# Kernel tuning notes

Measured on AMD Instinct MI355X. Metric: run time of the kernel, lower is better.

The kernel has to match this reference:

```python
import jax, jax.numpy as jnp
import numpy as np

HIDDEN = 1024
NUM_HEADS = 16
HEAD_DIM = HIDDEN // NUM_HEADS


def setup_inputs() -> dict:
    key = jax.random.key(0)
    ks = jax.random.split(key, 5)
    scale = 1.0 / np.sqrt(HIDDEN)
    x = jax.random.normal(ks[0], (2, 2048, HIDDEN), dtype=jnp.float32)
    qkv_w = jax.random.uniform(ks[1], (3 * HIDDEN, HIDDEN), jnp.float32, -scale, scale)
    qkv_b = jax.random.uniform(ks[2], (3 * HIDDEN,), jnp.float32, -scale, scale)
    out_w = jax.random.uniform(ks[3], (HIDDEN, HIDDEN), jnp.float32, -scale, scale)
    out_b = jax.random.uniform(ks[4], (HIDDEN,), jnp.float32, -scale, scale)
    return {"x": x, "qkv_w": qkv_w, "qkv_b": qkv_b, "out_w": out_w, "out_b": out_b}


def reference(x, qkv_w, qkv_b, out_w, out_b):
    B, S, _ = x.shape
    qkv = jnp.einsum('bsd,ed->bse', x, qkv_w) + qkv_b  # [B,S,3H]
    q, k, v = jnp.split(qkv, 3, axis=-1)
    # [B,S,H] -> [B,nh,S,hd]
    def to_heads(t):
        return t.reshape(B, S, NUM_HEADS, HEAD_DIM).transpose(0, 2, 1, 3)
    q, k, v = to_heads(q), to_heads(k), to_heads(v)
    scores = jnp.einsum('bhqd,bhkd->bhqk', q, k) / np.sqrt(HEAD_DIM).astype(np.float32)
    attn = jax.nn.softmax(scores, axis=-1)
    o = jnp.einsum('bhqk,bhkd->bhqd', attn, v)
    o = o.transpose(0, 2, 1, 3).reshape(B, S, HIDDEN)
    return jnp.einsum('bsd,ed->bse', o, out_w) + out_b
```

## Files before the change

kernel.cpp:

```cpp
#include <hip/hip_runtime.h>
#include <stdint.h>

typedef __bf16 bf16x8 __attribute__((ext_vector_type(8)));
typedef float  f32x4  __attribute__((ext_vector_type(4)));
typedef float  f32x16 __attribute__((ext_vector_type(16)));
typedef unsigned short u16;
typedef unsigned int   u32;

#define B_  2
#define S_  2048
#define H_  1024
#define NH_ 16
#define HD_ 64
#define QSCL 0.18033688011112042f

__device__ __forceinline__ u16 f2bf(float f) {
  u32 u = __builtin_bit_cast(u32, f);
  return (u16)((u + 0x7FFFu + ((u >> 16) & 1u)) >> 16);
}
__device__ __forceinline__ float ex2(float x) { return __builtin_amdgcn_exp2f(x); }
__device__ __forceinline__ u32 cvtpk(float lo, float hi) {
  u32 r; asm("v_cvt_pk_bf16_f32 %0, %1, %2" : "=v"(r) : "v"(lo), "v"(hi)); return r;
}
__device__ __forceinline__ void gload_lds16(const u16* g, u16* lds) {
  __builtin_amdgcn_global_load_lds(
      (__attribute__((address_space(1))) void*)(void*)g,
      (__attribute__((address_space(3))) void*)lds, 16, 0, 0);
}

__global__ void cvt_all(const float* __restrict__ a, const float* __restrict__ b,
                        const float* __restrict__ c, u16* __restrict__ oa,
                        u16* __restrict__ ob, u16* __restrict__ oc) {
  int i = blockIdx.x * 256 + threadIdx.x;
  const float4* src; ushort4* dst; int j;
  if (i < 1048576)      { src = (const float4*)a; dst = (ushort4*)oa; j = i; }
  else if (i < 1835008) { src = (const float4*)b; dst = (ushort4*)ob; j = i - 1048576; }
  else                  { src = (const float4*)c; dst = (ushort4*)oc; j = i - 1835008; }
  const float4 v = src[j];
  ushort4 o;
  o.x = f2bf(v.x); o.y = f2bf(v.y); o.z = f2bf(v.z); o.w = f2bf(v.w);
  dst[j] = o;
}

__global__ __launch_bounds__(256, 2)
void gemm_qkv(const u16* __restrict__ A, const u16* __restrict__ W,
              const float* __restrict__ bias,
              u16* __restrict__ qb, u16* __restrict__ kb, u16* __restrict__ vb,
              int M, int N, int K)
{
  __shared__ __align__(16) u16 As[2][128 * 32];
  __shared__ __align__(16) u16 Bs[2][128 * 32];
  const int tid = threadIdx.x;
  const int w = tid >> 6, l = tid & 63;
  const int lg = l >> 4, lr = l & 15;
  const int wr = w >> 1, wc = w & 1;
  const int tM = blockIdx.y * 128, tN = blockIdx.x * 128;

  f32x4 acc[4][4];
  const f32x4 z4 = {0.f, 0.f, 0.f, 0.f};
#pragma unroll
  for (int m = 0; m < 4; ++m)
#pragma unroll
    for (int n = 0; n < 4; ++n) acc[m][n] = z4;

  auto STG = [&](int buf, int k0) {
#pragma unroll
    for (int i = 0; i < 2; ++i) {
      const int ch = i * 256 + tid;
      const int row = ch >> 2, cc = (ch & 3) * 8;
      gload_lds16(A + (size_t)(tM + row) * K + k0 + cc, As[buf] + (size_t)(i * 256 + w * 64) * 8);
      gload_lds16(W + (size_t)(tN + row) * K + k0 + cc, Bs[buf] + (size_t)(i * 256 + w * 64) * 8);
    }
  };

  STG(0, 0);
  __syncthreads();

  for (int it = 0; it < K / 32; ++it) {
    const int cur = it & 1;
    if (it + 1 < K / 32) STG(cur ^ 1, (it + 1) * 32);
    bf16x8 af[4], bw[4];
#pragma unroll
    for (int m = 0; m < 4; ++m)
      af[m] = *(const bf16x8*)&As[cur][(wr * 64 + m * 16 + lr) * 32 + lg * 8];
#pragma unroll
    for (int n = 0; n < 4; ++n)
      bw[n] = *(const bf16x8*)&Bs[cur][(wc * 64 + n * 16 + lr) * 32 + lg * 8];
#pragma unroll
    for (int m = 0; m < 4; ++m)
#pragma unroll
      for (int n = 0; n < 4; ++n)
        acc[m][n] = __builtin_amdgcn_mfma_f32_16x16x32_bf16(af[m], bw[n], acc[m][n], 0, 0, 0);
    __syncthreads();
  }

#pragma unroll
  for (int n = 0; n < 4; ++n) {
    const int col = tN + wc * 64 + n * 16 + lr;
    const float bv = bias[col];
    const int t3 = col >> 10, rem = col & 1023;
    const int hh = rem >> 6, dd = rem & 63;
    const float sc = (t3 == 0) ? QSCL : 1.f;
    u16* dst = (t3 == 0) ? qb : (t3 == 1) ? kb : vb;
#pragma unroll
    for (int m = 0; m < 4; ++m)
#pragma unroll
      for (int r = 0; r < 4; ++r) {
        const int row = tM + wr * 64 + m * 16 + lg * 4 + r;
        const int bb = row >> 11, ss = row & 2047;
        dst[((size_t)(bb * NH_ + hh) * S_ + ss) * HD_ + dd] = f2bf((acc[m][n][r] + bv) * sc);
      }
  }
}

__global__ __launch_bounds__(256, 4)
void vtrans(const u16* __restrict__ vb, u16* __restrict__ vtb)
{
  __shared__ u16 Ls[64 * 65];
  const int t = threadIdx.x;
  const int bh = blockIdx.y;
  const int s0 = blockIdx.x * 64;
  const u16* src = vb + ((size_t)bh * S_ + s0) * HD_;
  const int d = t & 63, sy = t >> 6;
#pragma unroll
  for (int p = 0; p < 16; ++p) {
    const int s = p * 4 + sy;
    Ls[s * 65 + d] = src[(size_t)s * HD_ + d];
  }
  __syncthreads();
  const int s = t & 63, dy = t >> 6;
  u16* dst = vtb + (size_t)bh * HD_ * S_ + s0;
#pragma unroll
  for (int p = 0; p < 16; ++p) {
    const int dd = p * 4 + dy;
    dst[(size_t)dd * S_ + s] = Ls[s * 65 + dd];
  }
}

__global__ __launch_bounds__(256, 2)
void gemm_out(const u16* __restrict__ A, const u16* __restrict__ W,
              const float* __restrict__ bias, float* __restrict__ outf,
              int M, int N, int K)
{
  __shared__ __align__(16) u16 As[2][128 * 32];
  __shared__ __align__(16) u16 Bs[2][64 * 32];
  const int tid = threadIdx.x;
  const int w = tid >> 6, l = tid & 63;
  const int lg = l >> 4, lr = l & 15;
  const int tM = blockIdx.y * 128, tN = blockIdx.x * 64;

  f32x4 acc[2][4];
  const f32x4 z4 = {0.f, 0.f, 0.f, 0.f};
#pragma unroll
  for (int m = 0; m < 2; ++m)
#pragma unroll
    for (int n = 0; n < 4; ++n) acc[m][n] = z4;

  auto STG = [&](int buf, int k0) {
#pragma unroll
    for (int i = 0; i < 2; ++i) {
      const int ch = i * 256 + tid;
      const int row = ch >> 2, cc = (ch & 3) * 8;
      gload_lds16(A + (size_t)(tM + row) * K + k0 + cc, As[buf] + (size_t)(i * 256 + w * 64) * 8);
    }
    gload_lds16(W + (size_t)(tN + (tid >> 2)) * K + k0 + (tid & 3) * 8, Bs[buf] + (size_t)(w * 64) * 8);
  };

  STG(0, 0);
  __syncthreads();

  for (int it = 0; it < K / 32; ++it) {
    const int cur = it & 1;
    if (it + 1 < K / 32) STG(cur ^ 1, (it + 1) * 32);
    bf16x8 af[2], bw[4];
#pragma unroll
    for (int m = 0; m < 2; ++m)
      af[m] = *(const bf16x8*)&As[cur][(w * 32 + m * 16 + lr) * 32 + lg * 8];
#pragma unroll
    for (int n = 0; n < 4; ++n)
      bw[n] = *(const bf16x8*)&Bs[cur][(n * 16 + lr) * 32 + lg * 8];
#pragma unroll
    for (int m = 0; m < 2; ++m)
#pragma unroll
      for (int n = 0; n < 4; ++n)
        acc[m][n] = __builtin_amdgcn_mfma_f32_16x16x32_bf16(af[m], bw[n], acc[m][n], 0, 0, 0);
    __syncthreads();
  }

#pragma unroll
  for (int n = 0; n < 4; ++n) {
    const int col = tN + n * 16 + lr;
    const float bv = bias[col];
#pragma unroll
    for (int m = 0; m < 2; ++m)
#pragma unroll
      for (int r = 0; r < 4; ++r) {
        const int row = tM + w * 32 + m * 16 + lg * 4 + r;
        outf[(size_t)row * N + col] = acc[m][n][r] + bv;
      }
  }
}

__global__ __launch_bounds__(256, 2)
void attn_fwd(const u16* __restrict__ qb, const u16* __restrict__ kb,
              const u16* __restrict__ vtb, u16* __restrict__ ob)
{
  __shared__ __align__(16) u16 Kl[2][2][64 * 64];
  __shared__ __align__(16) u16 Vl[2][2][64 * 64];

  const int tid = threadIdx.x;
  const int w = tid >> 6, l = tid & 63;
  const int q32 = l & 31, hi = l >> 5;
  const int idx = blockIdx.x;
  const int bh = idx & 31, qt = idx >> 5;
  const int bb = bh >> 4, hh = bh & 15;
  const int q0 = qt * 128 + w * 32;

  bf16x8 qf[4];
#pragma unroll
  for (int ks = 0; ks < 4; ++ks)
    qf[ks] = *(const bf16x8*)&qb[((size_t)bh * S_ + q0 + q32) * HD_ + ks * 16 + hi * 8];

  const f32x16 z16 = {};
  f32x16 acc[2] = {z16, z16};
  float lrun = 0.f;

  const int srow = l >> 3;
  const int scol = ((l & 7) ^ srow) << 3;
  const u16* kbase = kb  + ((size_t)bh * S_  + w * 16 + srow) * HD_ + scol;
  const u16* vbase = vtb + ((size_t)bh * HD_ + w * 16 + srow) * S_  + scol;

  auto STAGE = [&](int buf, int t) {
#pragma unroll
    for (int s = 0; s < 2; ++s)
#pragma unroll
      for (int j = 0; j < 2; ++j) {
        gload_lds16(kbase + ((size_t)t * 128 + s * 64) * HD_ + j * 8 * HD_,
                    &Kl[buf][s][(w * 16 + j * 8) * 64]);
        gload_lds16(vbase + (size_t)t * 128 + s * 64 + j * 8 * S_,
                    &Vl[buf][s][(w * 16 + j * 8) * 64]);
      }
  };

  STAGE(0, 0);
  __syncthreads();

  const int sw = q32 & 7;

  auto SOFTMAX = [&](f32x16& st0, f32x16& st1, bf16x8* pa) {
#pragma unroll
    for (int kt = 0; kt < 2; ++kt) {
      const f32x16& stt = kt ? st1 : st0;
      float p[16];
#pragma unroll
      for (int r = 0; r < 16; ++r) p[r] = ex2(stt[r]);
#pragma unroll
      for (int g = 0; g < 4; ++g)
        lrun += (p[4 * g] + p[4 * g + 1]) + (p[4 * g + 2] + p[4 * g + 3]);
      u32 wk0[4], wk1[4];
#pragma unroll
      for (int g = 0; g < 4; ++g) {
        wk0[g] = cvtpk(p[4 * g], p[4 * g + 1]);
        wk1[g] = cvtpk(p[4 * g + 2], p[4 * g + 3]);
      }
#pragma unroll
      for (int k2 = 0; k2 < 2; ++k2) {
        u32 a0 = wk0[2 * k2], b0 = wk0[2 * k2 + 1];
        u32 a1 = wk1[2 * k2], b1 = wk1[2 * k2 + 1];
        asm volatile("v_permlane32_swap_b32 %0, %1" : "+v"(a0), "+v"(b0));
        asm volatile("v_permlane32_swap_b32 %0, %1" : "+v"(a1), "+v"(b1));
        uint4 wv = {a0, a1, b0, b1};
        pa[kt * 2 + k2] = __builtin_bit_cast(bf16x8, wv);
      }
    }
  };

  for (int t = 0; t < 16; ++t) {
    const int cur = t & 1;
    if (t + 1 < 16) STAGE(cur ^ 1, t + 1);

    f32x16 stA0 = z16, stA1 = z16, stB0 = z16, stB1 = z16;
    __builtin_amdgcn_s_setprio(1);
#pragma unroll
    for (int ks = 0; ks < 4; ++ks) {
      const int so = ((((ks << 1) | hi) ^ sw) << 3);
      const bf16x8 kfA0 = *(const bf16x8*)&Kl[cur][0][(q32) * 64 + so];
      const bf16x8 kfA1 = *(const bf16x8*)&Kl[cur][0][(32 + q32) * 64 + so];
      const bf16x8 kfB0 = *(const bf16x8*)&Kl[cur][1][(q32) * 64 + so];
      const bf16x8 kfB1 = *(const bf16x8*)&Kl[cur][1][(32 + q32) * 64 + so];
      stA0 = __builtin_amdgcn_mfma_f32_32x32x16_bf16(kfA0, qf[ks], stA0, 0, 0, 0);
      stA1 = __builtin_amdgcn_mfma_f32_32x32x16_bf16(kfA1, qf[ks], stA1, 0, 0, 0);
      stB0 = __builtin_amdgcn_mfma_f32_32x32x16_bf16(kfB0, qf[ks], stB0, 0, 0, 0);
      stB1 = __builtin_amdgcn_mfma_f32_32x32x16_bf16(kfB1, qf[ks], stB1, 0, 0, 0);
    }
    __builtin_amdgcn_s_setprio(0);

    bf16x8 pa[4];
    SOFTMAX(stA0, stA1, pa);
    __builtin_amdgcn_s_setprio(1);
#pragma unroll
    for (int dt = 0; dt < 2; ++dt)
#pragma unroll
      for (int ks = 0; ks < 4; ++ks) {
        const bf16x8 vf = *(const bf16x8*)&Vl[cur][0][(dt * 32 + q32) * 64 + ((((ks << 1) | hi) ^ sw) << 3)];
        acc[dt] = __builtin_amdgcn_mfma_f32_32x32x16_bf16(vf, pa[ks], acc[dt], 0, 0, 0);
      }
    __builtin_amdgcn_s_setprio(0);

    SOFTMAX(stB0, stB1, pa);
    __builtin_amdgcn_s_setprio(1);
#pragma unroll
    for (int dt = 0; dt < 2; ++dt)
#pragma unroll
      for (int ks = 0; ks < 4; ++ks) {
        const bf16x8 vf = *(const bf16x8*)&Vl[cur][1][(dt * 32 + q32) * 64 + ((((ks << 1) | hi) ^ sw) << 3)];
        acc[dt] = __builtin_amdgcn_mfma_f32_32x32x16_bf16(vf, pa[ks], acc[dt], 0, 0, 0);
      }
    __builtin_amdgcn_s_setprio(0);

    __syncthreads();
  }

  lrun += __shfl_xor(lrun, 32);
  const float linv = 1.f / lrun;
  const size_t orow = ((size_t)(bb * S_ + q0 + q32)) * H_ + hh * HD_;
#pragma unroll
  for (int dt = 0; dt < 2; ++dt)
#pragma unroll
    for (int g = 0; g < 4; ++g) {
      const u32 o0 = cvtpk(acc[dt][4 * g] * linv, acc[dt][4 * g + 1] * linv);
      const u32 o1 = cvtpk(acc[dt][4 * g + 2] * linv, acc[dt][4 * g + 3] * linv);
      uint2 ov; ov.x = o0; ov.y = o1;
      *(uint2*)&ob[orow + dt * 32 + g * 8 + hi * 4] = ov;
    }
}

extern "C" void kernel_launch(void* const* d_in, const int* in_sizes, int n_in,
                              void* d_out, int out_size, void* d_ws, size_t ws_size,
                              hipStream_t stream) {
  const float* x     = (const float*)d_in[0];
  const float* qkv_w = (const float*)d_in[1];
  const float* qkv_b = (const float*)d_in[2];
  const float* out_w = (const float*)d_in[3];
  const float* out_b = (const float*)d_in[4];

  char* ws = (char*)d_ws;
  u16* xb    = (u16*)(ws);
  u16* wqkvb = (u16*)(ws + 8388608);
  u16* wob   = (u16*)(ws + 14680064);
  u16* qb    = (u16*)(ws + 16777216);
  u16* kb    = (u16*)(ws + 25165824);
  u16* vb    = (u16*)(ws + 33554432);
  u16* ob    = (u16*)(ws + 41943040);
  u16* vtb   = xb;

  cvt_all<<<8192, 256, 0, stream>>>(x, qkv_w, out_w, xb, wqkvb, wob);

  gemm_qkv<<<dim3(24, 32), 256, 0, stream>>>(xb, wqkvb, qkv_b,
                                             qb, kb, vb, 4096, 3072, 1024);
  vtrans<<<dim3(32, 32), 256, 0, stream>>>(vb, vtb);
  attn_fwd<<<512, 256, 0, stream>>>(qb, kb, vtb, ob);
  gemm_out<<<dim3(16, 32), 256, 0, stream>>>(ob, wob, out_b, (float*)d_out,
                                             4096, 1024, 1024);
}
```

Before: 114.9 us.

## Restructure QKV GEMM with 256x192 tiles, XOR-swizzled LDS and interleaved prefetch

Rewrites the QKV projection GEMM to use 512-thread blocks computing 256x192 output tiles with a K-step of 64. The LDS layout is XOR-swizzled to avoid bank conflicts, and next-stage global->LDS loads are interleaved with the MFMA phases using raw s_barrier and s_setprio. The aim is more data reuse per tile, fewer LDS conflicts and better overlap of loads with math. The cost is more registers and LDS per block and a grid of 256 blocks, which may under-fill the CUs.

```diff
diff --git a/kernel.cpp b/kernel.cpp
--- a/kernel.cpp
+++ b/kernel.cpp
@@ -27,6 +27,7 @@
       (__attribute__((address_space(1))) void*)(void*)g,
       (__attribute__((address_space(3))) void*)lds, 16, 0, 0);
 }
+#define SBAR() asm volatile("s_barrier" ::: "memory")
 
 __global__ void cvt_all(const float* __restrict__ a, const float* __restrict__ b,
                         const float* __restrict__ c, u16* __restrict__ oa,
@@ -42,71 +43,100 @@
   dst[j] = o;
 }
 
-__global__ __launch_bounds__(256, 2)
+__global__ __launch_bounds__(512, 2)
 void gemm_qkv(const u16* __restrict__ A, const u16* __restrict__ W,
               const float* __restrict__ bias,
-              u16* __restrict__ qb, u16* __restrict__ kb, u16* __restrict__ vb,
-              int M, int N, int K)
+              u16* __restrict__ qb, u16* __restrict__ kb, u16* __restrict__ vb)
 {
-  __shared__ __align__(16) u16 As[2][128 * 32];
-  __shared__ __align__(16) u16 Bs[2][128 * 32];
+  __shared__ __align__(16) u16 Al[2][256 * 64];
+  __shared__ __align__(16) u16 Bl[2][192 * 64];
+  const int K = 1024;
   const int tid = threadIdx.x;
   const int w = tid >> 6, l = tid & 63;
   const int lg = l >> 4, lr = l & 15;
-  const int wr = w >> 1, wc = w & 1;
-  const int tM = blockIdx.y * 128, tN = blockIdx.x * 128;
-
-  f32x4 acc[4][4];
-  const f32x4 z4 = {0.f, 0.f, 0.f, 0.f};
-#pragma unroll
-  for (int m = 0; m < 4; ++m)
-#pragma unroll
-    for (int n = 0; n < 4; ++n) acc[m][n] = z4;
-
-  auto STG = [&](int buf, int k0) {
-#pragma unroll
-    for (int i = 0; i < 2; ++i) {
-      const int ch = i * 256 + tid;
-      const int row = ch >> 2, cc = (ch & 3) * 8;
-      gload_lds16(A + (size_t)(tM + row) * K + k0 + cc, As[buf] + (size_t)(i * 256 + w * 64) * 8);
-      gload_lds16(W + (size_t)(tN + row) * K + k0 + cc, Bs[buf] + (size_t)(i * 256 + w * 64) * 8);
-    }
-  };
-
-  STG(0, 0);
-  __syncthreads();
-
-  for (int it = 0; it < K / 32; ++it) {
-    const int cur = it & 1;
-    if (it + 1 < K / 32) STG(cur ^ 1, (it + 1) * 32);
-    bf16x8 af[4], bw[4];
-#pragma unroll
-    for (int m = 0; m < 4; ++m)
-      af[m] = *(const bf16x8*)&As[cur][(wr * 64 + m * 16 + lr) * 32 + lg * 8];
-#pragma unroll
-    for (int n = 0; n < 4; ++n)
-      bw[n] = *(const bf16x8*)&Bs[cur][(wc * 64 + n * 16 + lr) * 32 + lg * 8];
-#pragma unroll
-    for (int m = 0; m < 4; ++m)
-#pragma unroll
-      for (int n = 0; n < 4; ++n)
-        acc[m][n] = __builtin_amdgcn_mfma_f32_16x16x32_bf16(af[m], bw[n], acc[m][n], 0, 0, 0);
-    __syncthreads();
-  }
-
-#pragma unroll
-  for (int n = 0; n < 4; ++n) {
-    const int col = tN + wc * 64 + n * 16 + lr;
+  const int wm = w >> 2, wn = w & 3;
+  const int tM = blockIdx.y * 256, tN = blockIdx.x * 192;
+
+  f32x4 acc[8][3] = {};
+
+  const int srow = l >> 3;
+  const int scol = ((l & 7) ^ srow) << 3;
+  const u16* asrc = A + (size_t)(tM + w * 8 + srow) * K + scol;
+  const u16* bsrc = W + (size_t)(tN + w * 8 + srow) * K + scol;
+
+  auto STGA = [&](int buf, int k0, int j) {
+    gload_lds16(asrc + (size_t)j * 64 * K + k0, &Al[buf][(j * 64 + w * 8) * 64]);
+  };
+  auto STGB = [&](int buf, int k0, int j) {
+    gload_lds16(bsrc + (size_t)j * 64 * K + k0, &Bl[buf][(j * 64 + w * 8) * 64]);
+  };
+
+#pragma unroll
+  for (int j = 0; j < 4; ++j) STGA(0, 0, j);
+#pragma unroll
+  for (int j = 0; j < 3; ++j) STGB(0, 0, j);
+  asm volatile("s_waitcnt vmcnt(0)" ::: "memory");
+  SBAR();
+
+  const int sw = lr & 7;
+
+  for (int t = 0; t < 16; ++t) {
+    const int cur = t & 1, nb = cur ^ 1;
+    const int k1 = (t + 1) * 64;
+    const bool pre = (t + 1 < 16);
+
+    bf16x8 bw[3][2];
+
+#pragma unroll
+    for (int p = 0; p < 4; ++p) {
+      bf16x8 af[2][2];
+#pragma unroll
+      for (int m2 = 0; m2 < 2; ++m2)
+#pragma unroll
+        for (int kk = 0; kk < 2; ++kk)
+          af[m2][kk] = *(const bf16x8*)&Al[cur][(wm * 128 + (p * 2 + m2) * 16 + lr) * 64 +
+                                               (((kk * 4 + lg) ^ sw) << 3)];
+      if (p == 0) {
+#pragma unroll
+        for (int n = 0; n < 3; ++n)
+#pragma unroll
+          for (int kk = 0; kk < 2; ++kk)
+            bw[n][kk] = *(const bf16x8*)&Bl[cur][(wn * 48 + n * 16 + lr) * 64 +
+                                                (((kk * 4 + lg) ^ sw) << 3)];
+      }
+      if (pre) {
+        STGA(nb, k1, p);
+        if (p < 3) STGB(nb, k1, p);
+      }
+      SBAR();
+      __builtin_amdgcn_s_setprio(1);
+#pragma unroll
+      for (int m2 = 0; m2 < 2; ++m2)
+#pragma unroll
+        for (int n = 0; n < 3; ++n)
+#pragma unroll
+          for (int kk = 0; kk < 2; ++kk)
+            acc[p * 2 + m2][n] = __builtin_amdgcn_mfma_f32_16x16x32_bf16(
+                af[m2][kk], bw[n][kk], acc[p * 2 + m2][n], 0, 0, 0);
+      __builtin_amdgcn_s_setprio(0);
+      if (p == 3) asm volatile("s_waitcnt vmcnt(0)" ::: "memory");
+      SBAR();
+    }
+  }
+
+#pragma unroll
+  for (int n = 0; n < 3; ++n) {
+    const int col = tN + wn * 48 + n * 16 + lr;
     const float bv = bias[col];
     const int t3 = col >> 10, rem = col & 1023;
     const int hh = rem >> 6, dd = rem & 63;
     const float sc = (t3 == 0) ? QSCL : 1.f;
     u16* dst = (t3 == 0) ? qb : (t3 == 1) ? kb : vb;
 #pragma unroll
-    for (int m = 0; m < 4; ++m)
+    for (int m = 0; m < 8; ++m)
 #pragma unroll
       for (int r = 0; r < 4; ++r) {
-        const int row = tM + wr * 64 + m * 16 + lg * 4 + r;
+        const int row = tM + wm * 128 + m * 16 + lg * 4 + r;
         const int bb = row >> 11, ss = row & 2047;
         dst[((size_t)(bb * NH_ + hh) * S_ + ss) * HD_ + dd] = f2bf((acc[m][n][r] + bv) * sc);
       }
@@ -356,8 +386,7 @@
 
   cvt_all<<<8192, 256, 0, stream>>>(x, qkv_w, out_w, xb, wqkvb, wob);
 
-  gemm_qkv<<<dim3(24, 32), 256, 0, stream>>>(xb, wqkvb, qkv_b,
-                                             qb, kb, vb, 4096, 3072, 1024);
+  gemm_qkv<<<dim3(16, 16), 512, 0, stream>>>(xb, wqkvb, qkv_b, qb, kb, vb);
   vtrans<<<dim3(32, 32), 256, 0, stream>>>(vb, vtb);
   attn_fwd<<<512, 256, 0, stream>>>(qb, kb, vtb, ob);
   gemm_out<<<dim3(16, 32), 256, 0, stream>>>(ob, wob, out_b, (float*)d_out,
```

Result: no change. 114.9 us (+0.0%).

## Restructure QKV GEMM with 128x192x64 tiles, XOR-swizzled LDS and priority hints

Applied to the files above, without the earlier changes.

Reworks the QKV projection GEMM to use larger 128x192 output tiles with a 64-wide K step, halving the number of K iterations and barriers. LDS stores use an XOR swizzle on 16-byte chunks to avoid bank conflicts on fragment reads. Explicit vmcnt waits plus raw s_barrier replace __syncthreads, and s_setprio is raised around the MFMA block. The grid shrinks from 768 to 512 blocks, and each block uses more LDS and accumulator registers, which may lower occupancy.

```diff
diff --git a/kernel.cpp b/kernel.cpp
--- a/kernel.cpp
+++ b/kernel.cpp
@@ -27,6 +27,7 @@
       (__attribute__((address_space(1))) void*)(void*)g,
       (__attribute__((address_space(3))) void*)lds, 16, 0, 0);
 }
+#define SBAR() asm volatile("s_barrier" ::: "memory")
 
 __global__ void cvt_all(const float* __restrict__ a, const float* __restrict__ b,
                         const float* __restrict__ c, u16* __restrict__ oa,
@@ -45,58 +46,70 @@
 __global__ __launch_bounds__(256, 2)
 void gemm_qkv(const u16* __restrict__ A, const u16* __restrict__ W,
               const float* __restrict__ bias,
-              u16* __restrict__ qb, u16* __restrict__ kb, u16* __restrict__ vb,
-              int M, int N, int K)
+              u16* __restrict__ qb, u16* __restrict__ kb, u16* __restrict__ vb)
 {
-  __shared__ __align__(16) u16 As[2][128 * 32];
-  __shared__ __align__(16) u16 Bs[2][128 * 32];
+  __shared__ __align__(16) u16 Al[2][128 * 64];
+  __shared__ __align__(16) u16 Bl[2][192 * 64];
+  const int K = 1024;
   const int tid = threadIdx.x;
   const int w = tid >> 6, l = tid & 63;
   const int lg = l >> 4, lr = l & 15;
-  const int wr = w >> 1, wc = w & 1;
-  const int tM = blockIdx.y * 128, tN = blockIdx.x * 128;
-
-  f32x4 acc[4][4];
-  const f32x4 z4 = {0.f, 0.f, 0.f, 0.f};
-#pragma unroll
-  for (int m = 0; m < 4; ++m)
-#pragma unroll
-    for (int n = 0; n < 4; ++n) acc[m][n] = z4;
+  const int wm = w >> 1, wn = w & 1;
+  const int tM = blockIdx.y * 128, tN = blockIdx.x * 192;
+
+  f32x4 acc[4][6] = {};
+
+  const int srow = l >> 3;
+  const int scol = ((l & 7) ^ srow) << 3;
+  const u16* asrc = A + (size_t)(tM + w * 32 + srow) * K + scol;
+  const u16* bsrc = W + (size_t)(tN + w * 48 + srow) * K + scol;
 
   auto STG = [&](int buf, int k0) {
 #pragma unroll
-    for (int i = 0; i < 2; ++i) {
-      const int ch = i * 256 + tid;
-      const int row = ch >> 2, cc = (ch & 3) * 8;
-      gload_lds16(A + (size_t)(tM + row) * K + k0 + cc, As[buf] + (size_t)(i * 256 + w * 64) * 8);
-      gload_lds16(W + (size_t)(tN + row) * K + k0 + cc, Bs[buf] + (size_t)(i * 256 + w * 64) * 8);
-    }
+    for (int j = 0; j < 4; ++j)
+      gload_lds16(asrc + (size_t)(j * 8) * K + k0, &Al[buf][(w * 32 + j * 8) * 64]);
+#pragma unroll
+    for (int j = 0; j < 6; ++j)
+      gload_lds16(bsrc + (size_t)(j * 8) * K + k0, &Bl[buf][(w * 48 + j * 8) * 64]);
   };
 
   STG(0, 0);
-  __syncthreads();
-
-  for (int it = 0; it < K / 32; ++it) {
-    const int cur = it & 1;
-    if (it + 1 < K / 32) STG(cur ^ 1, (it + 1) * 32);
-    bf16x8 af[4], bw[4];
+  asm volatile("s_waitcnt vmcnt(0)" ::: "memory");
+  SBAR();
+
+  const int sw = lr & 7;
+
+  for (int t = 0; t < 16; ++t) {
+    const int cur = t & 1;
+    if (t + 1 < 16) STG(cur ^ 1, (t + 1) * 64);
+
+    bf16x8 af[4][2];
 #pragma unroll
     for (int m = 0; m < 4; ++m)
-      af[m] = *(const bf16x8*)&As[cur][(wr * 64 + m * 16 + lr) * 32 + lg * 8];
-#pragma unroll
-    for (int n = 0; n < 4; ++n)
-      bw[n] = *(const bf16x8*)&Bs[cur][(wc * 64 + n * 16 + lr) * 32 + lg * 8];
-#pragma unroll
-    for (int m = 0; m < 4; ++m)
-#pragma unroll
-      for (int n = 0; n < 4; ++n)
-        acc[m][n] = __builtin_amdgcn_mfma_f32_16x16x32_bf16(af[m], bw[n], acc[m][n], 0, 0, 0);
-    __syncthreads();
-  }
-
-#pragma unroll
-  for (int n = 0; n < 4; ++n) {
-    const int col = tN + wc * 64 + n * 16 + lr;
+#pragma unroll
+      for (int kk = 0; kk < 2; ++kk)
+        af[m][kk] = *(const bf16x8*)&Al[cur][(wm * 64 + m * 16 + lr) * 64 +
+                                            (((kk * 4 + lg) ^ sw) << 3)];
+    __builtin_amdgcn_s_setprio(1);
+#pragma unroll
+    for (int n = 0; n < 6; ++n) {
+      bf16x8 bw0 = *(const bf16x8*)&Bl[cur][(wn * 96 + n * 16 + lr) * 64 + (((lg) ^ sw) << 3)];
+      bf16x8 bw1 = *(const bf16x8*)&Bl[cur][(wn * 96 + n * 16 + lr) * 64 + (((4 + lg) ^ sw) << 3)];
+#pragma unroll
+      for (int m = 0; m < 4; ++m) {
+        acc[m][n] = __builtin_amdgcn_mfma_f32_16x16x32_bf16(af[m][0], bw0, acc[m][n], 0, 0, 0);
+        acc[m][n] = __builtin_amdgcn_mfma_f32_16x16x32_bf16(af[m][1], bw1, acc[m][n], 0, 0, 0);
+      }
+    }
+    __builtin_amdgcn_s_setprio(0);
+
+    asm volatile("s_waitcnt vmcnt(0)" ::: "memory");
+    SBAR();
+  }
+
+#pragma unroll
+  for (int n = 0; n < 6; ++n) {
+    const int col = tN + wn * 96 + n * 16 + lr;
     const float bv = bias[col];
     const int t3 = col >> 10, rem = col & 1023;
     const int hh = rem >> 6, dd = rem & 63;
@@ -106,7 +119,7 @@
     for (int m = 0; m < 4; ++m)
 #pragma unroll
       for (int r = 0; r < 4; ++r) {
-        const int row = tM + wr * 64 + m * 16 + lg * 4 + r;
+        const int row = tM + wm * 64 + m * 16 + lg * 4 + r;
         const int bb = row >> 11, ss = row & 2047;
         dst[((size_t)(bb * NH_ + hh) * S_ + ss) * HD_ + dd] = f2bf((acc[m][n][r] + bv) * sc);
       }
@@ -356,8 +369,7 @@
 
   cvt_all<<<8192, 256, 0, stream>>>(x, qkv_w, out_w, xb, wqkvb, wob);
 
-  gemm_qkv<<<dim3(24, 32), 256, 0, stream>>>(xb, wqkvb, qkv_b,
-                                             qb, kb, vb, 4096, 3072, 1024);
+  gemm_qkv<<<dim3(16, 32), 256, 0, stream>>>(xb, wqkvb, qkv_b, qb, kb, vb);
   vtrans<<<dim3(32, 32), 256, 0, stream>>>(vb, vtb);
   attn_fwd<<<512, 256, 0, stream>>>(qb, kb, vtb, ob);
   gemm_out<<<dim3(16, 32), 256, 0, stream>>>(ob, wob, out_b, (float*)d_out,
```

Result: faster. 109.5 us (-4.7%).
